# Optimization experiments

Hardware: AMD Instinct MI355X
Metric: run time of the kernel (lower is better)

## Reference

```python
import jax, jax.numpy as jnp
import numpy as np

N_NODES = 100000
N_EDGES = 1600000
IN_DIM, H1, H2, OUT_DIM = 128, 64, 64, 64


def _glorot(key, shape):
    fan_in, fan_out = shape
    lim = np.sqrt(6.0 / (fan_in + fan_out)).astype(np.float32)
    return jax.random.uniform(key, shape, jnp.float32, -lim, lim)


def setup_inputs() -> dict:
    key = jax.random.key(0)
    ks = jax.random.split(key, 8)
    x = jax.random.normal(ks[0], (N_NODES, IN_DIM), jnp.float32)
    edge_index = jax.random.randint(ks[1], (2, N_EDGES), 0, N_NODES, jnp.int64)
    W1 = _glorot(ks[2], (IN_DIM, H1))
    b1 = jnp.zeros((H1,), jnp.float32)
    W2 = _glorot(ks[3], (H1, H2))
    b2 = jnp.zeros((H2,), jnp.float32)
    Wfc = _glorot(ks[4], (H2, OUT_DIM))
    bfc = jnp.zeros((OUT_DIM,), jnp.float32)
    return {"x": x, "W1": W1, "b1": b1, "W2": W2, "b2": b2,
            "Wfc": Wfc, "bfc": bfc, "edge_index": edge_index}


def _gcn_conv(x, src, dst, dinv, W, b, n_nodes):
    # PyG GCNConv: h = D^{-1/2} (A + I) D^{-1/2} (x W) + b
    h = x @ W                                   # [N, out]
    norm = dinv[src] * dinv[dst]                # [E'] edge weights
    msg = norm[:, None] * h[src]                # gather + scale, [E', out]
    agg = jax.ops.segment_sum(msg, dst, num_segments=n_nodes)
    return agg + b


def reference(x, W1, b1, W2, b2, Wfc, bfc, edge_index):
    n = x.shape[0]
    loop = jnp.arange(n, dtype=edge_index.dtype)
    src = jnp.concatenate([edge_index[0], loop])   # self-loops appended
    dst = jnp.concatenate([edge_index[1], loop])
    deg = jnp.zeros((n,), x.dtype).at[dst].add(1.0)  # degree incl. self-loop
    dinv = jax.lax.rsqrt(deg)

    h = jax.nn.relu(_gcn_conv(x, src, dst, dinv, W1, b1, n))
    h = jax.nn.relu(_gcn_conv(h, src, dst, dinv, W2, b2, n))
    embedding = h
    logits = h @ Wfc + bfc
    return embedding, logits
```

## Files before the change

### kernel.cpp

```cpp
#include <hip/hip_runtime.h>
#include <hip/hip_bf16.h>


constexpr int IN_DIM  = 128;
constexpr int HDIM    = 64;
constexpr int NBLK_A  = 256;
constexpr int BSH     = 8;
constexpr int MAXNB   = 512;
constexpr int PADSLK  = 1792;

__device__ __forceinline__ float bf2f(unsigned int u) {
    return __uint_as_float(u << 16);
}
__device__ __forceinline__ unsigned short f2bf_bits(float f) {
    __hip_bfloat16 b = __float2bfloat16(f);
    return *(unsigned short*)&b;
}


__global__ void binA_count(const int* __restrict__ dst, int* __restrict__ histg,
                           int E, int NB, int chunk) {
    __shared__ int h[MAXNB];
    for (int i = threadIdx.x; i < NB; i += 256) h[i] = 0;
    __syncthreads();
    int beg = blockIdx.x * chunk;
    int end = min(E, beg + chunk);
    for (int e = beg + threadIdx.x; e < end; e += 256)
        atomicAdd(&h[dst[e] >> BSH], 1);
    __syncthreads();
    for (int i = threadIdx.x; i < NB; i += 256)
        histg[i * NBLK_A + blockIdx.x] = h[i];
}

__global__ void binA_scanblocks(int* __restrict__ histg, int* __restrict__ btot) {
    __shared__ int sm[NBLK_A];
    int tid = threadIdx.x;
    int v = histg[blockIdx.x * NBLK_A + tid];
    sm[tid] = v;
    __syncthreads();
    for (int off = 1; off < NBLK_A; off <<= 1) {
        int t = (tid >= off) ? sm[tid - off] : 0;
        __syncthreads();
        sm[tid] += t;
        __syncthreads();
    }
    histg[blockIdx.x * NBLK_A + tid] = sm[tid] - v;
    if (tid == NBLK_A - 1) btot[blockIdx.x] = sm[tid];
}

__device__ __forceinline__ void bucket_scan(const int* __restrict__ btot,
                                            int* bb, int NB) {
    int tid = threadIdx.x;
    for (int i = tid; i < MAXNB; i += 256) bb[i] = (i < NB) ? btot[i] : 0;
    __syncthreads();
    for (int off = 1; off < MAXNB; off <<= 1) {
        int i0 = tid, i1 = tid + 256;
        int t0 = (i0 >= off) ? bb[i0 - off] : 0;
        int t1 = (i1 >= off) ? bb[i1 - off] : 0;
        __syncthreads();
        bb[i0] += t0;
        bb[i1] += t1;
        __syncthreads();
    }
}

__global__ void binA_scatter(const int* __restrict__ src, const int* __restrict__ dst,
                             const int* __restrict__ histg, const int* __restrict__ btot,
                             int* __restrict__ staging, int E, int NB, int chunk) {
    __shared__ int bb[MAXNB];
    __shared__ int cur[MAXNB];
    bucket_scan(btot, bb, NB);
    for (int i = threadIdx.x; i < NB; i += 256)
        cur[i] = (bb[i] - btot[i]) + histg[i * NBLK_A + blockIdx.x];
    __syncthreads();
    int beg = blockIdx.x * chunk;
    int end = min(E, beg + chunk);
    for (int e = beg + threadIdx.x; e < end; e += 256) {
        int s = src[e];
        int d = dst[e];
        int pos = atomicAdd(&cur[d >> BSH], 1);
        staging[pos] = (s << BSH) | (d & 255);
    }
}

__global__ void binB_finalize(const int* __restrict__ staging, const int* __restrict__ btot,
                              int2* __restrict__ rows, int* __restrict__ esrc,
                              float* __restrict__ dinv, unsigned int* __restrict__ hp_rowN,
                              int N, int NB) {
    __shared__ int bb[MAXNB];
    __shared__ int cnt[256], sm[256], cur[256];
    int tid = threadIdx.x;
    int b = blockIdx.x;
    bucket_scan(btot, bb, NB);
    int node0 = b << BSH;
    int nloc = min(256, N - node0);
    int eend = bb[b];
    int ebeg = eend - btot[b];
    int ebegP = ebeg + b * PADSLK;
    cnt[tid] = 0;
    __syncthreads();
    for (int e = ebeg + tid; e < eend; e += 256)
        atomicAdd(&cnt[staging[e] & 255], 1);
    __syncthreads();
    int v = cnt[tid];
    int pv = (v + 7) & ~7;
    sm[tid] = pv;
    __syncthreads();
    for (int off = 1; off < 256; off <<= 1) {
        int t = (tid >= off) ? sm[tid - off] : 0;
        __syncthreads();
        sm[tid] += t;
        __syncthreads();
    }
    int excl = sm[tid] - pv;
    cur[tid] = excl;
    __syncthreads();
    if (tid < nloc) {
        rows[node0 + tid] = make_int2(ebegP + excl, ebegP + excl + pv);
        dinv[node0 + tid] = rsqrtf((float)v + 1.0f);
        for (int q = v; q < pv; ++q)
            esrc[ebegP + excl + q] = N;
    }
    if (b == 0 && tid < 32) hp_rowN[tid] = 0u;
    for (int e = ebeg + tid; e < eend; e += 256) {
        int p = staging[e];
        int pos = ebegP + atomicAdd(&cur[p & 255], 1);
        esrc[pos] = p >> BSH;
    }
}


template<int K, bool IBF16, bool SCALE, bool BIAS, bool OBF16>
__device__ __forceinline__ void gemm_body(
        const void* __restrict__ Xv, const float* __restrict__ W,
        const float* __restrict__ bias, const float* __restrict__ dinv,
        void* __restrict__ Yv, int n) {
    constexpr int KC = 32;
    constexpr int XSTR = 132;
    __shared__ float Xt[KC * XSTR];
    __shared__ float Ws[KC * 64];
    const int tid = threadIdx.x;
    const int node0 = blockIdx.x * 128;
    const int r0 = (tid >> 4) * 8;
    const int c0 = (tid & 15) * 4;

    float acc[8][4];
#pragma unroll
    for (int a = 0; a < 8; ++a)
#pragma unroll
        for (int b = 0; b < 4; ++b) acc[a][b] = 0.f;

    for (int kc = 0; kc < K; kc += KC) {
        __syncthreads();
#pragma unroll
        for (int i = 0; i < 4; ++i) {
            int s = tid + i * 256;
            int row = s >> 3;
            int kq = s & 7;
            int grow = node0 + row;
            float4 v = make_float4(0.f, 0.f, 0.f, 0.f);
            if (grow < n) {
                if (IBF16) {
                    uint2 u = *(const uint2*)&((const unsigned short*)Xv)[(size_t)grow * K + kc + kq * 4];
                    v.x = bf2f(u.x & 0xffff); v.y = bf2f(u.x >> 16);
                    v.z = bf2f(u.y & 0xffff); v.w = bf2f(u.y >> 16);
                } else {
                    v = *(const float4*)&((const float*)Xv)[(size_t)grow * K + kc + kq * 4];
                }
            }
            Xt[(kq * 4 + 0) * XSTR + row] = v.x;
            Xt[(kq * 4 + 1) * XSTR + row] = v.y;
            Xt[(kq * 4 + 2) * XSTR + row] = v.z;
            Xt[(kq * 4 + 3) * XSTR + row] = v.w;
        }
#pragma unroll
        for (int i = 0; i < 2; ++i) {
            int s = tid + i * 256;
            *(float4*)&Ws[s * 4] = *(const float4*)&W[(size_t)kc * 64 + s * 4];
        }
        __syncthreads();
#pragma unroll
        for (int kk = 0; kk < KC; kk += 4) {
            float4 xa[4][2];
            float4 wv[4];
#pragma unroll
            for (int i = 0; i < 4; ++i) {
                xa[i][0] = *(const float4*)&Xt[(kk + i) * XSTR + r0];
                xa[i][1] = *(const float4*)&Xt[(kk + i) * XSTR + r0 + 4];
                wv[i]    = *(const float4*)&Ws[(kk + i) * 64 + c0];
            }
#pragma unroll
            for (int i = 0; i < 4; ++i) {
                const float* xp = (const float*)&xa[i][0];
                const float* wp = (const float*)&wv[i];
#pragma unroll
                for (int rr = 0; rr < 8; ++rr)
#pragma unroll
                    for (int cc = 0; cc < 4; ++cc)
                        acc[rr][cc] += xp[rr] * wp[cc];
            }
        }
    }
#pragma unroll
    for (int rr = 0; rr < 8; ++rr) {
        int node = node0 + r0 + rr;
        if (node < n) {
            float d = SCALE ? dinv[node] : 1.0f;
            float t[4];
#pragma unroll
            for (int cc = 0; cc < 4; ++cc) {
                float v = acc[rr][cc];
                if (BIAS) v += bias[c0 + cc];
                t[cc] = v * d;
            }
            if (OBF16) {
                __hip_bfloat16 vb[4];
#pragma unroll
                for (int cc = 0; cc < 4; ++cc) vb[cc] = __float2bfloat16(t[cc]);
                *(uint2*)&((__hip_bfloat16*)Yv)[(size_t)node * 64 + c0] = *(uint2*)vb;
            } else {
                *(float4*)&((float*)Yv)[(size_t)node * 64 + c0] = *(float4*)t;
            }
        }
    }
}

__global__ __launch_bounds__(256, 4) void gemm1_kernel(
        const float* X, const float* W, const float* dinv, void* Y, int n) {
    gemm_body<IN_DIM, false, true, false, true>(X, W, nullptr, dinv, Y, n);
}
__global__ __launch_bounds__(256, 4) void gemm2_kernel(
        const void* X, const float* W, const float* dinv, void* Y, int n) {
    gemm_body<HDIM, true, true, false, true>(X, W, nullptr, dinv, Y, n);
}
__global__ __launch_bounds__(256, 4) void fc_kernel(
        const float* X, const float* W, const float* bias, void* Y, int n) {
    gemm_body<HDIM, false, false, true, false>(X, W, bias, nullptr, Y, n);
}

template<bool OBF16>
__global__ __launch_bounds__(256) void agg_kernel(
        const uint4* __restrict__ hp4, const int* __restrict__ esrc,
        const int2* __restrict__ rows, const float* __restrict__ dinv,
        const float* __restrict__ bias, void* __restrict__ out, int n) {
    const int lane = threadIdx.x & 63;
    const int j = lane & 7;
    const int step = gridDim.x * 32;
    for (int idx = blockIdx.x * 32 + (threadIdx.x >> 6) * 8 + (lane >> 3);
         idx < n; idx += step) {
        const int node = idx;
        const int2 be = rows[node];

        float acc[8];
        {
            uint4 u = hp4[(size_t)node * 8 + j];
            acc[0] = bf2f(u.x & 0xffff); acc[1] = bf2f(u.x >> 16);
            acc[2] = bf2f(u.y & 0xffff); acc[3] = bf2f(u.y >> 16);
            acc[4] = bf2f(u.z & 0xffff); acc[5] = bf2f(u.z >> 16);
            acc[6] = bf2f(u.w & 0xffff); acc[7] = bf2f(u.w >> 16);
        }
        int k = be.x;
        for (; k + 16 <= be.y; k += 16) {
            int s[16];
#pragma unroll
            for (int i = 0; i < 16; ++i)
                s[i] = __builtin_nontemporal_load(&esrc[k + i]);
            uint4 u[16];
#pragma unroll
            for (int i = 0; i < 16; ++i)
                u[i] = hp4[(size_t)s[i] * 8 + j];
#pragma unroll
            for (int i = 0; i < 16; ++i) {
                acc[0] += bf2f(u[i].x & 0xffff); acc[1] += bf2f(u[i].x >> 16);
                acc[2] += bf2f(u[i].y & 0xffff); acc[3] += bf2f(u[i].y >> 16);
                acc[4] += bf2f(u[i].z & 0xffff); acc[5] += bf2f(u[i].z >> 16);
                acc[6] += bf2f(u[i].w & 0xffff); acc[7] += bf2f(u[i].w >> 16);
            }
        }
        if (k < be.y) {
            int s[8];
#pragma unroll
            for (int i = 0; i < 8; ++i)
                s[i] = __builtin_nontemporal_load(&esrc[k + i]);
            uint4 u[8];
#pragma unroll
            for (int i = 0; i < 8; ++i)
                u[i] = hp4[(size_t)s[i] * 8 + j];
#pragma unroll
            for (int i = 0; i < 8; ++i) {
                acc[0] += bf2f(u[i].x & 0xffff); acc[1] += bf2f(u[i].x >> 16);
                acc[2] += bf2f(u[i].y & 0xffff); acc[3] += bf2f(u[i].y >> 16);
                acc[4] += bf2f(u[i].z & 0xffff); acc[5] += bf2f(u[i].z >> 16);
                acc[6] += bf2f(u[i].w & 0xffff); acc[7] += bf2f(u[i].w >> 16);
            }
        }
        const float d = dinv[node];
        float o[8];
#pragma unroll
        for (int t = 0; t < 8; ++t)
            o[t] = fmaxf(fmaf(d, acc[t], bias[8 * j + t]), 0.f);

        if (OBF16) {
            uint4 pk;
            pk.x = (unsigned)f2bf_bits(o[0]) | ((unsigned)f2bf_bits(o[1]) << 16);
            pk.y = (unsigned)f2bf_bits(o[2]) | ((unsigned)f2bf_bits(o[3]) << 16);
            pk.z = (unsigned)f2bf_bits(o[4]) | ((unsigned)f2bf_bits(o[5]) << 16);
            pk.w = (unsigned)f2bf_bits(o[6]) | ((unsigned)f2bf_bits(o[7]) << 16);
            ((uint4*)out)[(size_t)node * 8 + j] = pk;
        } else {
            ((float4*)out)[(size_t)node * 16 + 2 * j]     = make_float4(o[0], o[1], o[2], o[3]);
            ((float4*)out)[(size_t)node * 16 + 2 * j + 1] = make_float4(o[4], o[5], o[6], o[7]);
        }
    }
}

extern "C" void kernel_launch(void* const* d_in, const int* in_sizes, int n_in,
                              void* d_out, int out_size, void* d_ws, size_t ws_size,
                              hipStream_t stream) {
    const float* x   = (const float*)d_in[0];
    const float* W1  = (const float*)d_in[1];
    const float* b1  = (const float*)d_in[2];
    const float* W2  = (const float*)d_in[3];
    const float* b2  = (const float*)d_in[4];
    const float* Wfc = (const float*)d_in[5];
    const float* bfc = (const float*)d_in[6];
    const int*  eidx = (const int*)d_in[7];

    const int N = in_sizes[0] / IN_DIM;
    const int E = in_sizes[7] / 2;
    const int* src = eidx;
    const int* dst = eidx + E;

    const int NB    = (N + 255) >> BSH;
    const int chunk = (E + NBLK_A - 1) / NBLK_A;
    const int EP    = E + NB * PADSLK;

    int* p = (int*)d_ws;
    int2* rows = (int2*)p;           p += (size_t)2 * N + 2;
    float* dinv = (float*)p;         p += (size_t)((N + 3) & ~3);
    int* histg = p;                  p += (size_t)((NB * NBLK_A + 3) & ~3);
    int* btot = p;                   p += 512;
    int* esrc = p;                   p += (size_t)((EP + 3) & ~3);
    unsigned short* hp = (unsigned short*)p;   p += (size_t)(N + 1) * 32;
    unsigned short* h1 = (unsigned short*)p;   p += (size_t)N * 32;
    int* staging = (int*)hp;
    unsigned int* hp_rowN = (unsigned int*)(hp + (size_t)N * 64);

    float* emb    = (float*)d_out;
    float* logits = emb + (size_t)N * HDIM;

    binA_count<<<NBLK_A, 256, 0, stream>>>(dst, histg, E, NB, chunk);
    binA_scanblocks<<<NB, NBLK_A, 0, stream>>>(histg, btot);
    binA_scatter<<<NBLK_A, 256, 0, stream>>>(src, dst, histg, btot, staging, E, NB, chunk);
    binB_finalize<<<NB, 256, 0, stream>>>(staging, btot, rows, esrc, dinv, hp_rowN, N, NB);

    const int gBlocks = (N + 127) / 128;
    const int aBlocks = 2048;

    gemm1_kernel<<<gBlocks, 256, 0, stream>>>(x, W1, dinv, hp, N);
    agg_kernel<true><<<aBlocks, 256, 0, stream>>>(
        (const uint4*)hp, esrc, rows, dinv, b1, h1, N);

    gemm2_kernel<<<gBlocks, 256, 0, stream>>>(h1, W2, dinv, hp, N);
    agg_kernel<false><<<aBlocks, 256, 0, stream>>>(
        (const uint4*)hp, esrc, rows, dinv, b2, emb, N);

    fc_kernel<<<gBlocks, 256, 0, stream>>>(emb, Wfc, bfc, logits, N);
}
```

Baseline: 314.8 us.

## Replace FP32 SIMT GEMMs with bf16 MFMA matrix-core GEMMs

The three dense GEMM kernels (layer1, layer2, fc) now stage a 64-row tile of X and the transposed weight matrix into LDS as bf16 and compute with mfma_f32_16x16x32_bf16, one 16-row strip per wavefront. Outputs go through an LDS staging area so they can be written back as coalesced 16-byte stores. This replaces scalar FMA outer-product work with matrix-core instructions. The trade-off is lower precision: fp32 x and the fc input are now rounded to bf16, and every block re-converts the weights.

```diff
diff --git a/kernel.cpp b/kernel.cpp
--- a/kernel.cpp
+++ b/kernel.cpp
@@ -8,6 +8,9 @@
 constexpr int BSH     = 8;
 constexpr int MAXNB   = 512;
 constexpr int PADSLK  = 1792;
+
+typedef short bf16x8 __attribute__((ext_vector_type(8)));
+typedef float f32x4  __attribute__((ext_vector_type(4)));
 
 __device__ __forceinline__ float bf2f(unsigned int u) {
     return __uint_as_float(u << 16);
@@ -129,114 +132,126 @@
     }
 }
 
-
 template<int K, bool IBF16, bool SCALE, bool BIAS, bool OBF16>
-__device__ __forceinline__ void gemm_body(
+__device__ __forceinline__ void mfma_gemm_body(
         const void* __restrict__ Xv, const float* __restrict__ W,
         const float* __restrict__ bias, const float* __restrict__ dinv,
         void* __restrict__ Yv, int n) {
-    constexpr int KC = 32;
-    constexpr int XSTR = 132;
-    __shared__ float Xt[KC * XSTR];
-    __shared__ float Ws[KC * 64];
+    constexpr int STR = K + 8;
+    __shared__ short SMEM[2 * 64 * STR];
+    __shared__ float dls[64];
+    short* At = SMEM;
+    short* Wt = SMEM + 64 * STR;
     const int tid = threadIdx.x;
-    const int node0 = blockIdx.x * 128;
-    const int r0 = (tid >> 4) * 8;
-    const int c0 = (tid & 15) * 4;
-
-    float acc[8][4];
-#pragma unroll
-    for (int a = 0; a < 8; ++a)
-#pragma unroll
-        for (int b = 0; b < 4; ++b) acc[a][b] = 0.f;
-
-    for (int kc = 0; kc < K; kc += KC) {
-        __syncthreads();
+    const int node0 = blockIdx.x * 64;
+    const int w = tid >> 6;
+    const int lane = tid & 63;
+    const int lrow = lane & 15;
+    const int khal = lane >> 4;
+
+    if (IBF16) {
+#pragma unroll
+        for (int i = 0; i < K / 32; ++i) {
+            int s = tid + i * 256;
+            int row = s >> 3, j = s & 7;
+            int grow = node0 + row;
+            uint4 u = make_uint4(0, 0, 0, 0);
+            if (grow < n)
+                u = *(const uint4*)&((const unsigned short*)Xv)[(size_t)grow * K + j * 8];
+            *(uint4*)&At[row * STR + j * 8] = u;
+        }
+    } else {
+#pragma unroll
+        for (int i = 0; i < K / 16; ++i) {
+            int s = tid + i * 256;
+            int row = s / (K / 4), kq = s % (K / 4);
+            int grow = node0 + row;
+            float4 v = make_float4(0.f, 0.f, 0.f, 0.f);
+            if (grow < n)
+                v = *(const float4*)&((const float*)Xv)[(size_t)grow * K + kq * 4];
+            unsigned short pk[4] = {f2bf_bits(v.x), f2bf_bits(v.y),
+                                    f2bf_bits(v.z), f2bf_bits(v.w)};
+            *(uint2*)&At[row * STR + kq * 4] = *(uint2*)pk;
+        }
+    }
+#pragma unroll
+    for (int i = 0; i < K / 4; ++i) {
+        int s = tid + i * 256;
+        int k = s >> 6, c = s & 63;
+        Wt[c * STR + k] = (short)f2bf_bits(W[s]);
+    }
+    if (SCALE && tid < 64)
+        dls[tid] = (node0 + tid < n) ? dinv[node0 + tid] : 1.0f;
+    __syncthreads();
+
+    f32x4 acc[4];
+#pragma unroll
+    for (int ct = 0; ct < 4; ++ct)
+#pragma unroll
+        for (int r = 0; r < 4; ++r) acc[ct][r] = 0.f;
+#pragma unroll
+    for (int kt = 0; kt < K / 32; ++kt) {
+        int k0 = kt * 32 + khal * 8;
+        bf16x8 a = *(bf16x8*)&At[(w * 16 + lrow) * STR + k0];
+#pragma unroll
+        for (int ct = 0; ct < 4; ++ct) {
+            bf16x8 b = *(bf16x8*)&Wt[(ct * 16 + lrow) * STR + k0];
+            acc[ct] = __builtin_amdgcn_mfma_f32_16x16x32_bf16(a, b, acc[ct], 0, 0, 0);
+        }
+    }
+    __syncthreads();
+
+    short* Ot = SMEM;
+    float* Of = (float*)SMEM;
+#pragma unroll
+    for (int ct = 0; ct < 4; ++ct) {
+#pragma unroll
+        for (int r = 0; r < 4; ++r) {
+            int row = w * 16 + khal * 4 + r;
+            int col = ct * 16 + lrow;
+            float v = acc[ct][r];
+            if (BIAS) v += bias[col];
+            if (SCALE) v *= dls[row];
+            if (OBF16) Ot[row * 72 + col] = (short)f2bf_bits(v);
+            else       Of[row * 68 + col] = v;
+        }
+    }
+    __syncthreads();
+
+    if (OBF16) {
+#pragma unroll
+        for (int i = 0; i < 2; ++i) {
+            int s = tid + i * 256;
+            int row = s >> 3, j = s & 7;
+            if (node0 + row < n)
+                *(uint4*)&((unsigned short*)Yv)[(size_t)(node0 + row) * 64 + j * 8] =
+                    *(uint4*)&Ot[row * 72 + j * 8];
+        }
+    } else {
 #pragma unroll
         for (int i = 0; i < 4; ++i) {
             int s = tid + i * 256;
-            int row = s >> 3;
-            int kq = s & 7;
-            int grow = node0 + row;
-            float4 v = make_float4(0.f, 0.f, 0.f, 0.f);
-            if (grow < n) {
-                if (IBF16) {
-                    uint2 u = *(const uint2*)&((const unsigned short*)Xv)[(size_t)grow * K + kc + kq * 4];
-                    v.x = bf2f(u.x & 0xffff); v.y = bf2f(u.x >> 16);
-                    v.z = bf2f(u.y & 0xffff); v.w = bf2f(u.y >> 16);
-                } else {
-                    v = *(const float4*)&((const float*)Xv)[(size_t)grow * K + kc + kq * 4];
-                }
-            }
-            Xt[(kq * 4 + 0) * XSTR + row] = v.x;
-            Xt[(kq * 4 + 1) * XSTR + row] = v.y;
-            Xt[(kq * 4 + 2) * XSTR + row] = v.z;
-            Xt[(kq * 4 + 3) * XSTR + row] = v.w;
-        }
-#pragma unroll
-        for (int i = 0; i < 2; ++i) {
-            int s = tid + i * 256;
-            *(float4*)&Ws[s * 4] = *(const float4*)&W[(size_t)kc * 64 + s * 4];
-        }
-        __syncthreads();
-#pragma unroll
-        for (int kk = 0; kk < KC; kk += 4) {
-            float4 xa[4][2];
-            float4 wv[4];
-#pragma unroll
-            for (int i = 0; i < 4; ++i) {
-                xa[i][0] = *(const float4*)&Xt[(kk + i) * XSTR + r0];
-                xa[i][1] = *(const float4*)&Xt[(kk + i) * XSTR + r0 + 4];
-                wv[i]    = *(const float4*)&Ws[(kk + i) * 64 + c0];
-            }
-#pragma unroll
-            for (int i = 0; i < 4; ++i) {
-                const float* xp = (const float*)&xa[i][0];
-                const float* wp = (const float*)&wv[i];
-#pragma unroll
-                for (int rr = 0; rr < 8; ++rr)
-#pragma unroll
-                    for (int cc = 0; cc < 4; ++cc)
-                        acc[rr][cc] += xp[rr] * wp[cc];
-            }
-        }
-    }
-#pragma unroll
-    for (int rr = 0; rr < 8; ++rr) {
-        int node = node0 + r0 + rr;
-        if (node < n) {
-            float d = SCALE ? dinv[node] : 1.0f;
-            float t[4];
-#pragma unroll
-            for (int cc = 0; cc < 4; ++cc) {
-                float v = acc[rr][cc];
-                if (BIAS) v += bias[c0 + cc];
-                t[cc] = v * d;
-            }
-            if (OBF16) {
-                __hip_bfloat16 vb[4];
-#pragma unroll
-                for (int cc = 0; cc < 4; ++cc) vb[cc] = __float2bfloat16(t[cc]);
-                *(uint2*)&((__hip_bfloat16*)Yv)[(size_t)node * 64 + c0] = *(uint2*)vb;
-            } else {
-                *(float4*)&((float*)Yv)[(size_t)node * 64 + c0] = *(float4*)t;
-            }
-        }
-    }
-}
-
-__global__ __launch_bounds__(256, 4) void gemm1_kernel(
+            int row = s >> 4, q = s & 15;
+            if (node0 + row < n)
+                *(float4*)&((float*)Yv)[(size_t)(node0 + row) * 64 + q * 4] =
+                    *(float4*)&Of[row * 68 + q * 4];
+        }
+    }
+}
+
+__global__ __launch_bounds__(256, 4) void mgemm1_kernel(
         const float* X, const float* W, const float* dinv, void* Y, int n) {
-    gemm_body<IN_DIM, false, true, false, true>(X, W, nullptr, dinv, Y, n);
-}
-__global__ __launch_bounds__(256, 4) void gemm2_kernel(
+    mfma_gemm_body<IN_DIM, false, true, false, true>(X, W, nullptr, dinv, Y, n);
+}
+__global__ __launch_bounds__(256, 4) void mgemm2_kernel(
         const void* X, const float* W, const float* dinv, void* Y, int n) {
-    gemm_body<HDIM, true, true, false, true>(X, W, nullptr, dinv, Y, n);
-}
-__global__ __launch_bounds__(256, 4) void fc_kernel(
+    mfma_gemm_body<HDIM, true, true, false, true>(X, W, nullptr, dinv, Y, n);
+}
+__global__ __launch_bounds__(256, 4) void mfc_kernel(
         const float* X, const float* W, const float* bias, void* Y, int n) {
-    gemm_body<HDIM, false, false, true, false>(X, W, bias, nullptr, Y, n);
-}
+    mfma_gemm_body<HDIM, false, false, true, false>(X, W, bias, nullptr, Y, n);
+}
+
 
 template<bool OBF16>
 __global__ __launch_bounds__(256) void agg_kernel(
@@ -354,16 +369,16 @@
     binA_scatter<<<NBLK_A, 256, 0, stream>>>(src, dst, histg, btot, staging, E, NB, chunk);
     binB_finalize<<<NB, 256, 0, stream>>>(staging, btot, rows, esrc, dinv, hp_rowN, N, NB);
 
-    const int gBlocks = (N + 127) / 128;
+    const int mB = (N + 63) / 64;
     const int aBlocks = 2048;
 
-    gemm1_kernel<<<gBlocks, 256, 0, stream>>>(x, W1, dinv, hp, N);
+    mgemm1_kernel<<<mB, 256, 0, stream>>>(x, W1, dinv, hp, N);
     agg_kernel<true><<<aBlocks, 256, 0, stream>>>(
         (const uint4*)hp, esrc, rows, dinv, b1, h1, N);
 
-    gemm2_kernel<<<gBlocks, 256, 0, stream>>>(h1, W2, dinv, hp, N);
+    mgemm2_kernel<<<mB, 256, 0, stream>>>(h1, W2, dinv, hp, N);
     agg_kernel<false><<<aBlocks, 256, 0, stream>>>(
         (const uint4*)hp, esrc, rows, dinv, b2, emb, N);
 
-    fc_kernel<<<gBlocks, 256, 0, stream>>>(emb, Wfc, bfc, logits, N);
-}
+    mfc_kernel<<<mB, 256, 0, stream>>>(emb, Wfc, bfc, logits, N);
+}
```

Measured after the change: 286.9 us. 1.1x faster.
